# Kernel optimization log

Hardware: AMD Instinct MI355X
Metric: run time of the kernel (lower is better)

Reference implementation:

```python
import jax, jax.numpy as jnp
import numpy as np

N_SRC0, N_DST0 = 200000, 50000
N_DST1 = 10000
D_IN, D_HID = 128, 128


def _sage_mean(h, src, dst, n_dst, W_self, b_self, W_neigh, b_neigh, act):
    # gather messages from src nodes, mean-aggregate per dst node
    msg = h[src]                                             # [E, D]
    agg = jax.ops.segment_sum(msg, dst, num_segments=n_dst)  # [n_dst, D]
    deg = jax.ops.segment_sum(jnp.ones(dst.shape, h.dtype), dst, num_segments=n_dst)
    h_neigh = agg / jnp.maximum(deg, 1.0)[:, None]
    # DGL block convention: dst nodes are the first n_dst src nodes
    rst = h[:n_dst] @ W_self + b_self + h_neigh @ W_neigh + b_neigh
    return jax.nn.relu(rst) if act else rst


def setup_inputs() -> dict:
    key = jax.random.key(0)
    ks = jax.random.split(key, 12)
    s = 1.0 / np.sqrt(D_HID)
    return {
        "features": jax.random.normal(ks[0], (N_SRC0, D_IN), jnp.float32),
        "src0": jax.random.randint(ks[1], (800000,), 0, N_SRC0),
        "dst0": jax.random.randint(ks[2], (800000,), 0, N_DST0),
        "src1": jax.random.randint(ks[3], (160000,), 0, N_DST0),
        "dst1": jax.random.randint(ks[4], (160000,), 0, N_DST1),
        "W_init": jax.random.uniform(ks[5], (D_IN, D_HID), jnp.float32, -s, s),
        "b_init": jax.random.uniform(ks[6], (D_HID,), jnp.float32, -s, s),
        "W_self": jax.random.uniform(ks[7], (D_HID, D_HID), jnp.float32, -s, s),
        "b_self": jax.random.uniform(ks[8], (D_HID,), jnp.float32, -s, s),
        "W_neigh": jax.random.uniform(ks[9], (D_HID, D_HID), jnp.float32, -s, s),
        "b_neigh": jax.random.uniform(ks[10], (D_HID,), jnp.float32, -s, s),
    }


def reference(features, src0, dst0, src1, dst1, W_init, b_init, W_self, b_self, W_neigh, b_neigh):
    # fc_init + activation
    h = jax.nn.relu(features @ W_init + b_init)              # [N_SRC0, D_HID]
    # block 0 (act_flag True), dropout p=0.0 is identity
    h = _sage_mean(h, src0, dst0, N_DST0, W_self, b_self, W_neigh, b_neigh, act=True)
    # block 1 (last block: act_flag False)
    h = _sage_mean(h, src1, dst1, N_DST1, W_self, b_self, W_neigh, b_neigh, act=False)
    return jnp.squeeze(h, axis=1) if h.shape[1] == 1 else h  # h.squeeze(1) no-op for D_HID>1
```

## Files before the change

kernel.cpp:

```cpp
#include <hip/hip_runtime.h>
#include <stdint.h>
#include <stddef.h>


#define DIM 128
constexpr int N_SRC0 = 200000;
constexpr int N_DST0 = 50000;
constexpr int N_DST1 = 10000;
constexpr int E0 = 800000;
constexpr int E1 = 160000;
constexpr int MAXDEG = 64;

typedef __attribute__((ext_vector_type(8))) short bf16x8;
typedef __attribute__((ext_vector_type(4))) float f32x4;

__device__ __forceinline__ uint16_t f2bf(float f) {
  union { float f; uint32_t u; } v; v.f = f;
  return (uint16_t)((v.u + 0x7FFFu + ((v.u >> 16) & 1u)) >> 16);
}
__device__ __forceinline__ float bf2f(uint16_t h) {
  union { uint32_t u; float f; } v; v.u = ((uint32_t)h) << 16;
  return v.f;
}

__global__ __launch_bounds__(512) void prep_w_kernel(
    const float* __restrict__ W0, const float* __restrict__ W1,
    const float* __restrict__ W2, uint16_t* __restrict__ Wf) {
  int gid = blockIdx.x * 512 + threadIdx.x;
  if (gid >= 3 * 16384) return;
  int m = gid >> 14, idx = gid & 16383;
  const float* W = m == 0 ? W0 : (m == 1 ? W1 : W2);
  int j = idx & 7, lane = (idx >> 3) & 63, nt = (idx >> 9) & 7, kc = idx >> 12;
  int k = kc * 32 + (lane >> 4) * 8 + j;
  int n = nt * 16 + (lane & 15);
  Wf[gid] = f2bf(W[k * DIM + n]);
}

__global__ __launch_bounds__(256) void fc_init_kernel(
    const float* __restrict__ feat, const uint16_t* __restrict__ Wf,
    const float* __restrict__ bias, uint16_t* __restrict__ hout) {
  __shared__ uint16_t wl[16384];
  {
    const uint4* g = (const uint4*)Wf;
    uint4* s = (uint4*)wl;
    for (int i = threadIdx.x; i < 2048; i += 256) s[i] = g[i];
  }
  __syncthreads();

  int wave = (blockIdx.x * 256 + threadIdx.x) >> 6;
  int nwaves = (gridDim.x * 256) >> 6;
  int lane = threadIdx.x & 63;
  int q = lane >> 4, m16 = lane & 15;

  float bv[8];
#pragma unroll
  for (int nt = 0; nt < 8; nt++) bv[nt] = bias[nt * 16 + m16];

  const int nstrips = N_SRC0 / 16;
  for (int s = wave; s < nstrips; s += nwaves) {
    int m0 = s * 16;
    f32x4 acc[8];
#pragma unroll
    for (int nt = 0; nt < 8; nt++) acc[nt] = (f32x4){0.f, 0.f, 0.f, 0.f};

#pragma unroll
    for (int kc = 0; kc < 4; kc++) {
      const float* ap = feat + (size_t)(m0 + m16) * DIM + kc * 32 + q * 8;
      float4 x0 = *(const float4*)ap;
      float4 x1 = *(const float4*)(ap + 4);
      float xs[8] = {x0.x, x0.y, x0.z, x0.w, x1.x, x1.y, x1.z, x1.w};
      bf16x8 a;
#pragma unroll
      for (int j = 0; j < 8; j++) a[j] = (short)f2bf(xs[j]);
#pragma unroll
      for (int nt = 0; nt < 8; nt++) {
        bf16x8 w = *(const bf16x8*)&wl[(size_t)((kc * 8 + nt) * 64 + lane) * 8];
        acc[nt] = __builtin_amdgcn_mfma_f32_16x16x32_bf16(a, w, acc[nt], 0, 0, 0);
      }
    }
#pragma unroll
    for (int nt = 0; nt < 8; nt++)
#pragma unroll
      for (int r = 0; r < 4; r++) {
        float v = fmaxf(acc[nt][r] + bv[nt], 0.f);
        hout[(size_t)(m0 + q * 4 + r) * DIM + nt * 16 + m16] = f2bf(v);
      }
  }
}

__global__ __launch_bounds__(256) void place_kernel(
    const int* __restrict__ src, const int* __restrict__ dst, int E,
    int* __restrict__ cnt, int* __restrict__ eslot) {
  int i = blockIdx.x * 256 + threadIdx.x;
  if (i >= E) return;
  int d = dst[i];
  int p = atomicAdd(&cnt[d], 1);
  if (p < MAXDEG) eslot[(size_t)d * MAXDEG + p] = src[i];
}

__global__ __launch_bounds__(256) void agg_kernel(
    const int* __restrict__ eslot, const int* __restrict__ deg,
    const uint16_t* __restrict__ hsrc, uint16_t* __restrict__ hout, int n_dst) {
  int d = (blockIdx.x * 256 + threadIdx.x) >> 6;
  int lane = threadIdx.x & 63;
  if (d >= n_dst) return;
  const int* sl = eslot + (size_t)d * MAXDEG;
  int dg = deg[d];
  int dgc = dg < MAXDEG ? dg : MAXDEG;
  float a0 = 0.f, a1 = 0.f;
  int e = 0;
  for (; e + 4 <= dgc; e += 4) {
    int s0 = sl[e], s1 = sl[e + 1], s2 = sl[e + 2], s3 = sl[e + 3];
    uint32_t p0 = *(const uint32_t*)(hsrc + (size_t)s0 * DIM + lane * 2);
    uint32_t p1 = *(const uint32_t*)(hsrc + (size_t)s1 * DIM + lane * 2);
    uint32_t p2 = *(const uint32_t*)(hsrc + (size_t)s2 * DIM + lane * 2);
    uint32_t p3 = *(const uint32_t*)(hsrc + (size_t)s3 * DIM + lane * 2);
    a0 += bf2f((uint16_t)p0) + bf2f((uint16_t)p1) + bf2f((uint16_t)p2) + bf2f((uint16_t)p3);
    a1 += bf2f((uint16_t)(p0 >> 16)) + bf2f((uint16_t)(p1 >> 16)) +
          bf2f((uint16_t)(p2 >> 16)) + bf2f((uint16_t)(p3 >> 16));
  }
  for (; e < dgc; e++) {
    uint32_t p = *(const uint32_t*)(hsrc + (size_t)sl[e] * DIM + lane * 2);
    a0 += bf2f((uint16_t)p);
    a1 += bf2f((uint16_t)(p >> 16));
  }
  float inv = 1.f / fmaxf((float)dg, 1.f);
  uint32_t o = (uint32_t)f2bf(a0 * inv) | ((uint32_t)f2bf(a1 * inv) << 16);
  *(uint32_t*)(hout + (size_t)d * DIM + lane * 2) = o;
}

template <bool ACT, bool OUT_BF16>
__global__ __launch_bounds__(256) void sage_kernel(
    const uint16_t* __restrict__ hself, const uint16_t* __restrict__ hneigh,
    const uint16_t* __restrict__ WfS, const uint16_t* __restrict__ WfN,
    const float* __restrict__ bS, const float* __restrict__ bN,
    void* __restrict__ outp, int n_dst) {
  __shared__ uint16_t wS[16384];
  __shared__ uint16_t wN[16384];
  {
    const uint4* gS = (const uint4*)WfS;
    const uint4* gN = (const uint4*)WfN;
    uint4* sS = (uint4*)wS;
    uint4* sN = (uint4*)wN;
    for (int i = threadIdx.x; i < 2048; i += 256) { sS[i] = gS[i]; sN[i] = gN[i]; }
  }
  __syncthreads();

  int wave = (blockIdx.x * 256 + threadIdx.x) >> 6;
  int nwaves = (gridDim.x * 256) >> 6;
  int lane = threadIdx.x & 63;
  int q = lane >> 4, m16 = lane & 15;

  float bv[8];
#pragma unroll
  for (int nt = 0; nt < 8; nt++)
    bv[nt] = bS[nt * 16 + m16] + bN[nt * 16 + m16];

  const int nstrips = n_dst / 16;
  for (int s = wave; s < nstrips; s += nwaves) {
    int m0 = s * 16;
    f32x4 acc[8];
#pragma unroll
    for (int nt = 0; nt < 8; nt++) acc[nt] = (f32x4){0.f, 0.f, 0.f, 0.f};

#pragma unroll
    for (int kc = 0; kc < 4; kc++) {
      bf16x8 aS = *(const bf16x8*)(hself + (size_t)(m0 + m16) * DIM + kc * 32 + q * 8);
      bf16x8 aN = *(const bf16x8*)(hneigh + (size_t)(m0 + m16) * DIM + kc * 32 + q * 8);
#pragma unroll
      for (int nt = 0; nt < 8; nt++) {
        size_t fo = (size_t)((kc * 8 + nt) * 64 + lane) * 8;
        bf16x8 ws = *(const bf16x8*)&wS[fo];
        bf16x8 wn = *(const bf16x8*)&wN[fo];
        acc[nt] = __builtin_amdgcn_mfma_f32_16x16x32_bf16(aS, ws, acc[nt], 0, 0, 0);
        acc[nt] = __builtin_amdgcn_mfma_f32_16x16x32_bf16(aN, wn, acc[nt], 0, 0, 0);
      }
    }
#pragma unroll
    for (int nt = 0; nt < 8; nt++)
#pragma unroll
      for (int r = 0; r < 4; r++) {
        float v = acc[nt][r] + bv[nt];
        if (ACT) v = fmaxf(v, 0.f);
        size_t o = (size_t)(m0 + q * 4 + r) * DIM + nt * 16 + m16;
        if (OUT_BF16) ((uint16_t*)outp)[o] = f2bf(v);
        else          ((float*)outp)[o] = v;
      }
  }
}

extern "C" void kernel_launch(void* const* d_in, const int* in_sizes, int n_in,
                              void* d_out, int out_size, void* d_ws, size_t ws_size,
                              hipStream_t stream) {
  const float* feat   = (const float*)d_in[0];
  const int* src0     = (const int*)d_in[1];
  const int* dst0     = (const int*)d_in[2];
  const int* src1     = (const int*)d_in[3];
  const int* dst1     = (const int*)d_in[4];
  const float* W_init = (const float*)d_in[5];
  const float* b_init = (const float*)d_in[6];
  const float* W_self = (const float*)d_in[7];
  const float* b_self = (const float*)d_in[8];
  const float* W_neigh= (const float*)d_in[9];
  const float* b_neigh= (const float*)d_in[10];

  char* ws = (char*)d_ws;
  uint16_t* h    = (uint16_t*)(ws + 0);
  uint16_t* h1   = (uint16_t*)(ws + 51200000);
  uint16_t* hn   = (uint16_t*)(ws + 64000000);
  int*      cnt0 = (int*)(ws + 76800000);
  int*      cnt1 = (int*)(ws + 77000000);
  int*      eslot= (int*)(ws + 77040000);
  uint16_t* WfI  = (uint16_t*)(ws + 89840000);
  uint16_t* WfS  = WfI + 16384;
  uint16_t* WfN  = WfS + 16384;

  hipMemsetAsync(cnt0, 0, 240000, stream);
  prep_w_kernel<<<96, 512, 0, stream>>>(W_init, W_self, W_neigh, WfI);
  place_kernel<<<(E0 + 255) / 256, 256, 0, stream>>>(src0, dst0, E0, cnt0, eslot);

  fc_init_kernel<<<1024, 256, 0, stream>>>(feat, WfI, b_init, h);

  agg_kernel<<<N_DST0 / 4, 256, 0, stream>>>(eslot, cnt0, h, hn, N_DST0);
  sage_kernel<true, true><<<512, 256, 0, stream>>>(h, hn, WfS, WfN, b_self, b_neigh,
                                                   h1, N_DST0);

  place_kernel<<<(E1 + 255) / 256, 256, 0, stream>>>(src1, dst1, E1, cnt1, eslot);
  agg_kernel<<<N_DST1 / 4, 256, 0, stream>>>(eslot, cnt1, h1, hn, N_DST1);
  sage_kernel<false, false><<<160, 256, 0, stream>>>(h1, hn, WfS, WfN, b_self, b_neigh,
                                                     d_out, N_DST1);
}
```

Measured before the change: 326.5 us.

## Fuse memset and edge placement launches, prefetch next strip in GEMM kernels

Folds the count-buffer memset into the weight-prep kernel and merges both layers' edge placement into one launch using separate slot buffers, which removes a memset and a kernel launch. fc_init and sage kernels now software-pipeline their row loads, fetching the next strip's activations while the current strip's MFMAs run, and the fc_init grid is reduced. This raises register pressure and needs a second eslot workspace region.

Measured after the change: 313.5 us. 1.04x faster.

```diff
diff --git a/kernel.cpp b/kernel.cpp
--- a/kernel.cpp
+++ b/kernel.cpp
@@ -25,15 +25,37 @@
 
 __global__ __launch_bounds__(512) void prep_w_kernel(
     const float* __restrict__ W0, const float* __restrict__ W1,
-    const float* __restrict__ W2, uint16_t* __restrict__ Wf) {
+    const float* __restrict__ W2, uint16_t* __restrict__ Wf,
+    int* __restrict__ cnt, int ncnt) {
   int gid = blockIdx.x * 512 + threadIdx.x;
-  if (gid >= 3 * 16384) return;
-  int m = gid >> 14, idx = gid & 16383;
-  const float* W = m == 0 ? W0 : (m == 1 ? W1 : W2);
-  int j = idx & 7, lane = (idx >> 3) & 63, nt = (idx >> 9) & 7, kc = idx >> 12;
-  int k = kc * 32 + (lane >> 4) * 8 + j;
-  int n = nt * 16 + (lane & 15);
-  Wf[gid] = f2bf(W[k * DIM + n]);
+  if (gid < 3 * 16384) {
+    int m = gid >> 14, idx = gid & 16383;
+    const float* W = m == 0 ? W0 : (m == 1 ? W1 : W2);
+    int j = idx & 7, lane = (idx >> 3) & 63, nt = (idx >> 9) & 7, kc = idx >> 12;
+    int k = kc * 32 + (lane >> 4) * 8 + j;
+    int n = nt * 16 + (lane & 15);
+    Wf[gid] = f2bf(W[k * DIM + n]);
+  }
+  int z = gid - 3 * 16384;
+  if (z >= 0 && z < ncnt) cnt[z] = 0;
+}
+
+__global__ __launch_bounds__(256) void place_kernel(
+    const int* __restrict__ src0, const int* __restrict__ dst0,
+    const int* __restrict__ src1, const int* __restrict__ dst1,
+    int* __restrict__ cnt0, int* __restrict__ cnt1,
+    int* __restrict__ eslot0, int* __restrict__ eslot1) {
+  int i = blockIdx.x * 256 + threadIdx.x;
+  if (i < E0) {
+    int d = dst0[i];
+    int p = atomicAdd(&cnt0[d], 1);
+    if (p < MAXDEG) eslot0[(size_t)d * MAXDEG + p] = src0[i];
+  } else if (i - E0 < E1) {
+    int j = i - E0;
+    int d = dst1[j];
+    int p = atomicAdd(&cnt1[d], 1);
+    if (p < MAXDEG) eslot1[(size_t)d * MAXDEG + p] = src1[j];
+  }
 }
 
 __global__ __launch_bounds__(256) void fc_init_kernel(
@@ -57,18 +79,37 @@
   for (int nt = 0; nt < 8; nt++) bv[nt] = bias[nt * 16 + m16];
 
   const int nstrips = N_SRC0 / 16;
-  for (int s = wave; s < nstrips; s += nwaves) {
-    int m0 = s * 16;
+  int s = wave;
+  float4 X[8];
+  if (s < nstrips) {
+    const float* ap = feat + (size_t)(s * 16 + m16) * DIM + q * 8;
+#pragma unroll
+    for (int kc = 0; kc < 4; kc++) {
+      X[2 * kc]     = *(const float4*)(ap + kc * 32);
+      X[2 * kc + 1] = *(const float4*)(ap + kc * 32 + 4);
+    }
+  }
+
+  while (s < nstrips) {
+    int sn = s + nwaves;
+    float4 Y[8];
+    if (sn < nstrips) {
+      const float* ap = feat + (size_t)(sn * 16 + m16) * DIM + q * 8;
+#pragma unroll
+      for (int kc = 0; kc < 4; kc++) {
+        Y[2 * kc]     = *(const float4*)(ap + kc * 32);
+        Y[2 * kc + 1] = *(const float4*)(ap + kc * 32 + 4);
+      }
+    }
+
     f32x4 acc[8];
 #pragma unroll
     for (int nt = 0; nt < 8; nt++) acc[nt] = (f32x4){0.f, 0.f, 0.f, 0.f};
 
 #pragma unroll
     for (int kc = 0; kc < 4; kc++) {
-      const float* ap = feat + (size_t)(m0 + m16) * DIM + kc * 32 + q * 8;
-      float4 x0 = *(const float4*)ap;
-      float4 x1 = *(const float4*)(ap + 4);
-      float xs[8] = {x0.x, x0.y, x0.z, x0.w, x1.x, x1.y, x1.z, x1.w};
+      float xs[8] = {X[2 * kc].x, X[2 * kc].y, X[2 * kc].z, X[2 * kc].w,
+                     X[2 * kc + 1].x, X[2 * kc + 1].y, X[2 * kc + 1].z, X[2 * kc + 1].w};
       bf16x8 a;
 #pragma unroll
       for (int j = 0; j < 8; j++) a[j] = (short)f2bf(xs[j]);
@@ -78,6 +119,8 @@
         acc[nt] = __builtin_amdgcn_mfma_f32_16x16x32_bf16(a, w, acc[nt], 0, 0, 0);
       }
     }
+
+    int m0 = s * 16;
 #pragma unroll
     for (int nt = 0; nt < 8; nt++)
 #pragma unroll
@@ -85,17 +128,11 @@
         float v = fmaxf(acc[nt][r] + bv[nt], 0.f);
         hout[(size_t)(m0 + q * 4 + r) * DIM + nt * 16 + m16] = f2bf(v);
       }
-  }
-}
-
-__global__ __launch_bounds__(256) void place_kernel(
-    const int* __restrict__ src, const int* __restrict__ dst, int E,
-    int* __restrict__ cnt, int* __restrict__ eslot) {
-  int i = blockIdx.x * 256 + threadIdx.x;
-  if (i >= E) return;
-  int d = dst[i];
-  int p = atomicAdd(&cnt[d], 1);
-  if (p < MAXDEG) eslot[(size_t)d * MAXDEG + p] = src[i];
+
+#pragma unroll
+    for (int i = 0; i < 8; i++) X[i] = Y[i];
+    s = sn;
+  }
 }
 
 __global__ __launch_bounds__(256) void agg_kernel(
@@ -157,25 +194,46 @@
     bv[nt] = bS[nt * 16 + m16] + bN[nt * 16 + m16];
 
   const int nstrips = n_dst / 16;
-  for (int s = wave; s < nstrips; s += nwaves) {
-    int m0 = s * 16;
+  int s = wave;
+  bf16x8 XS[4], XN[4];
+  if (s < nstrips) {
+    size_t ro = (size_t)(s * 16 + m16) * DIM + q * 8;
+#pragma unroll
+    for (int kc = 0; kc < 4; kc++) {
+      XS[kc] = *(const bf16x8*)(hself + ro + kc * 32);
+      XN[kc] = *(const bf16x8*)(hneigh + ro + kc * 32);
+    }
+  }
+
+  while (s < nstrips) {
+    int sn = s + nwaves;
+    bf16x8 YS[4], YN[4];
+    if (sn < nstrips) {
+      size_t ro = (size_t)(sn * 16 + m16) * DIM + q * 8;
+#pragma unroll
+      for (int kc = 0; kc < 4; kc++) {
+        YS[kc] = *(const bf16x8*)(hself + ro + kc * 32);
+        YN[kc] = *(const bf16x8*)(hneigh + ro + kc * 32);
+      }
+    }
+
     f32x4 acc[8];
 #pragma unroll
     for (int nt = 0; nt < 8; nt++) acc[nt] = (f32x4){0.f, 0.f, 0.f, 0.f};
 
 #pragma unroll
     for (int kc = 0; kc < 4; kc++) {
-      bf16x8 aS = *(const bf16x8*)(hself + (size_t)(m0 + m16) * DIM + kc * 32 + q * 8);
-      bf16x8 aN = *(const bf16x8*)(hneigh + (size_t)(m0 + m16) * DIM + kc * 32 + q * 8);
 #pragma unroll
       for (int nt = 0; nt < 8; nt++) {
         size_t fo = (size_t)((kc * 8 + nt) * 64 + lane) * 8;
         bf16x8 ws = *(const bf16x8*)&wS[fo];
         bf16x8 wn = *(const bf16x8*)&wN[fo];
-        acc[nt] = __builtin_amdgcn_mfma_f32_16x16x32_bf16(aS, ws, acc[nt], 0, 0, 0);
-        acc[nt] = __builtin_amdgcn_mfma_f32_16x16x32_bf16(aN, wn, acc[nt], 0, 0, 0);
-      }
-    }
+        acc[nt] = __builtin_amdgcn_mfma_f32_16x16x32_bf16(XS[kc], ws, acc[nt], 0, 0, 0);
+        acc[nt] = __builtin_amdgcn_mfma_f32_16x16x32_bf16(XN[kc], wn, acc[nt], 0, 0, 0);
+      }
+    }
+
+    int m0 = s * 16;
 #pragma unroll
     for (int nt = 0; nt < 8; nt++)
 #pragma unroll
@@ -186,6 +244,10 @@
         if (OUT_BF16) ((uint16_t*)outp)[o] = f2bf(v);
         else          ((float*)outp)[o] = v;
       }
+
+#pragma unroll
+    for (int i = 0; i < 4; i++) { XS[i] = YS[i]; XN[i] = YN[i]; }
+    s = sn;
   }
 }
 
@@ -205,28 +267,28 @@
   const float* b_neigh= (const float*)d_in[10];
 
   char* ws = (char*)d_ws;
-  uint16_t* h    = (uint16_t*)(ws + 0);
-  uint16_t* h1   = (uint16_t*)(ws + 51200000);
-  uint16_t* hn   = (uint16_t*)(ws + 64000000);
-  int*      cnt0 = (int*)(ws + 76800000);
-  int*      cnt1 = (int*)(ws + 77000000);
-  int*      eslot= (int*)(ws + 77040000);
-  uint16_t* WfI  = (uint16_t*)(ws + 89840000);
-  uint16_t* WfS  = WfI + 16384;
-  uint16_t* WfN  = WfS + 16384;
-
-  hipMemsetAsync(cnt0, 0, 240000, stream);
-  prep_w_kernel<<<96, 512, 0, stream>>>(W_init, W_self, W_neigh, WfI);
-  place_kernel<<<(E0 + 255) / 256, 256, 0, stream>>>(src0, dst0, E0, cnt0, eslot);
-
-  fc_init_kernel<<<1024, 256, 0, stream>>>(feat, WfI, b_init, h);
-
-  agg_kernel<<<N_DST0 / 4, 256, 0, stream>>>(eslot, cnt0, h, hn, N_DST0);
+  uint16_t* h     = (uint16_t*)(ws + 0);
+  uint16_t* h1    = (uint16_t*)(ws + 51200000);
+  uint16_t* hn    = (uint16_t*)(ws + 64000000);
+  int*      cnt0  = (int*)(ws + 76800000);
+  int*      cnt1  = (int*)(ws + 77000000);
+  int*      eslot0= (int*)(ws + 77040000);
+  int*      eslot1= (int*)(ws + 89840000);
+  uint16_t* WfI   = (uint16_t*)(ws + 92400000);
+  uint16_t* WfS   = WfI + 16384;
+  uint16_t* WfN   = WfS + 16384;
+
+  prep_w_kernel<<<214, 512, 0, stream>>>(W_init, W_self, W_neigh, WfI, cnt0, 60000);
+  place_kernel<<<(E0 + E1 + 255) / 256, 256, 0, stream>>>(
+      src0, dst0, src1, dst1, cnt0, cnt1, eslot0, eslot1);
+
+  fc_init_kernel<<<768, 256, 0, stream>>>(feat, WfI, b_init, h);
+
+  agg_kernel<<<N_DST0 / 4, 256, 0, stream>>>(eslot0, cnt0, h, hn, N_DST0);
   sage_kernel<true, true><<<512, 256, 0, stream>>>(h, hn, WfS, WfN, b_self, b_neigh,
                                                    h1, N_DST0);
 
-  place_kernel<<<(E1 + 255) / 256, 256, 0, stream>>>(src1, dst1, E1, cnt1, eslot);
-  agg_kernel<<<N_DST1 / 4, 256, 0, stream>>>(eslot, cnt1, h1, hn, N_DST1);
+  agg_kernel<<<N_DST1 / 4, 256, 0, stream>>>(eslot1, cnt1, h1, hn, N_DST1);
   sage_kernel<false, false><<<160, 256, 0, stream>>>(h1, hn, WfS, WfN, b_self, b_neigh,
                                                      d_out, N_DST1);
 }
```
